# Kernel tuning notes

Measured on AMD Instinct MI355X. Metric: run time of the kernel, lower is better.

Reference implementation:

```python
import jax, jax.numpy as jnp
import numpy as np

NUM_STATES = 4096
NUM_OBS = 128
SEQ_LEN = 1024


def setup_inputs() -> dict:
    key = jax.random.key(0)
    kA, kB, kpi, kobs = jax.random.split(key, 4)
    # Scale A by 1/sqrt(N) so the forward recursion is numerically stable
    # (norm-preserving matvec); this only changes the random parameter draw,
    # not the math of the module.
    A = jax.random.normal(kA, (NUM_STATES, NUM_STATES), dtype=jnp.float32) / np.sqrt(NUM_STATES).astype(np.float32)
    B = jax.random.normal(kB, (NUM_STATES, NUM_OBS), dtype=jnp.float32)
    pi = jax.random.normal(kpi, (NUM_STATES,), dtype=jnp.float32)
    obs = jax.random.randint(kobs, (SEQ_LEN,), 0, NUM_OBS, dtype=jnp.int64)
    return {"A": A, "B": B, "pi": pi, "obs": obs}


def reference(A, B, pi, obs):
    # Gather the emission column for every timestep up front: (T, N)
    Bo = B[:, obs].T
    alpha0 = pi * Bo[0]  # (N,)

    def step(alpha, b_t):
        # alpha @ A : (N,) contracted with (N, N) -> (N,), then elementwise emission
        return (alpha @ A) * b_t, None

    alpha, _ = jax.lax.scan(step, alpha0, Bo[1:])
    return alpha.sum()
```

## Files before the change

kernel.cpp:

```cpp
#include <hip/hip_runtime.h>

constexpr int NSTATE = 4096;
constexpr int NOBS   = 128;
constexpr int TSEQ   = 1024;
constexpr int NWG    = 256;
constexpr int NTHR   = 1024;

constexpr size_t WS_BT    = 0;
constexpr size_t WS_OBS   = (size_t)NOBS * NSTATE;
constexpr size_t WS_FLAGS = WS_OBS + TSEQ;
constexpr size_t WS_Y2E   = WS_FLAGS + 512;

constexpr int XPAD = 20;

__device__ __forceinline__ int agent_ld_i32(const int* p) {
  return __hip_atomic_load(p, __ATOMIC_RELAXED, __HIP_MEMORY_SCOPE_AGENT);
}
__device__ __forceinline__ void agent_st_i32(int* p, int v) {
  __hip_atomic_store(p, v, __ATOMIC_RELAXED, __HIP_MEMORY_SCOPE_AGENT);
}
__device__ __forceinline__ void agent_st_f32(float* p, float v) {
  __hip_atomic_store(p, v, __ATOMIC_RELAXED, __HIP_MEMORY_SCOPE_AGENT);
}
__device__ __forceinline__ unsigned long long agent_ld_u64(const unsigned long long* p) {
  return __hip_atomic_load(p, __ATOMIC_RELAXED, __HIP_MEMORY_SCOPE_AGENT);
}
__device__ __forceinline__ void agent_st_u64(unsigned long long* p, unsigned long long v) {
  __hip_atomic_store(p, v, __ATOMIC_RELAXED, __HIP_MEMORY_SCOPE_AGENT);
}

__device__ __forceinline__ void grid_bar_full(int* flags, int w, int tid, int epoch) {
  asm volatile("s_waitcnt vmcnt(0)" ::: "memory");
  __syncthreads();
  if (tid == 0) agent_st_i32(&flags[w], epoch);
  if (tid < 64) {
    for (;;) {
      int m0 = agent_ld_i32(&flags[tid]);
      int m1 = agent_ld_i32(&flags[tid + 64]);
      int m2 = agent_ld_i32(&flags[tid + 128]);
      int m3 = agent_ld_i32(&flags[tid + 192]);
      int mn = min(min(m0, m1), min(m2, m3));
      if (__all(mn >= epoch)) break;
    }
  }
  __syncthreads();
}

__global__ __launch_bounds__(NTHR, 4) void hmm_fwd_kernel(
    const float* __restrict__ A,
    const float* __restrict__ B,
    const float* __restrict__ pi,
    const void*  __restrict__ obs_raw,
    float* __restrict__ out,
    float* __restrict__ ws)
{
  const int tid = threadIdx.x;
  const int w   = blockIdx.x;

  float* __restrict__ Bt    = ws + WS_BT;
  int*   __restrict__ obsg  = (int*)(ws + WS_OBS);
  int*   __restrict__ flags = (int*)(ws + WS_FLAGS);
  unsigned long long* __restrict__ y2e = (unsigned long long*)(ws + WS_Y2E);

  __shared__ float  x_lds[256 * XPAD];
  __shared__ float4 red_f[2][16][4];
  __shared__ int    obs_lds[TSEQ];
  __shared__ float  fin[16];
  __shared__ int    flag_lds;

  const int c4   = tid & 3;
  const int rg   = tid >> 2;
  const int ibase = rg << 4;
  const int col0  = (w << 4) + (c4 << 2);
  const int wave = tid >> 6;
  const int lane = tid & 63;

  const float* __restrict__ Abase = A + (size_t)ibase * NSTATE + col0;
  float ar[64];
#pragma unroll
  for (int k = 0; k < 16; ++k) {
    const float4 v = *(const float4*)(Abase + (size_t)k * NSTATE);
    ar[4*k+0] = v.x; ar[4*k+1] = v.y; ar[4*k+2] = v.z; ar[4*k+3] = v.w;
  }
#pragma unroll
  for (int i = 0; i < 64; ++i) asm volatile("" : "+v"(ar[i]));

  for (int e = w * NTHR + tid; e < NOBS * NSTATE; e += NWG * NTHR) {
    const int o = e >> 12;
    const int j = e & (NSTATE - 1);
    agent_st_f32(&Bt[(size_t)o * NSTATE + j], B[(size_t)j * NOBS + o]);
  }
  if (w == 0) {
    if (tid == 0) flag_lds = 0;
    __syncthreads();
    const long long* p64 = (const long long*)obs_raw;
    if (tid < 256) {
      const long long v = p64[tid];
      if (v < 0 || v >= NOBS) atomicOr(&flag_lds, 1);
    }
    __syncthreads();
    const bool is32 = (flag_lds != 0);
    const int* p32 = (const int*)obs_raw;
    agent_st_i32(&obsg[tid], is32 ? p32[tid] : (int)p64[tid]);
  }
  if (tid < 16) {
    union { float f; unsigned u; } cv;
    cv.f = pi[(w << 4) + tid];
    agent_st_u64(&y2e[(w << 4) + tid], (unsigned long long)cv.u);
  }
  grid_bar_full(flags, w, tid, 1);

  obs_lds[tid] = obsg[tid];
  __syncthreads();

  for (int t = 1; t < TSEQ; ++t) {
    const int bufc = (t - 1) & 1;
    const int bufp = t & 1;
    const int tagc = t - 1;
    const int o = obs_lds[t - 1];

    {
      const float4 bb = ((const float4*)(Bt + ((size_t)o << 12)))[tid];
      const unsigned long long* src = &y2e[(size_t)bufc * NSTATE + 4 * tid];
      unsigned long long v0, v1, v2, v3;
      for (;;) {
        v0 = agent_ld_u64(src + 0); v1 = agent_ld_u64(src + 1);
        v2 = agent_ld_u64(src + 2); v3 = agent_ld_u64(src + 3);
        bool ok = ((int)(v0 >> 32) == tagc) & ((int)(v1 >> 32) == tagc)
                & ((int)(v2 >> 32) == tagc) & ((int)(v3 >> 32) == tagc);
        if (ok) break;
      }
      union { unsigned u; float f; } e0, e1, e2, e3;
      e0.u = (unsigned)v0; e1.u = (unsigned)v1;
      e2.u = (unsigned)v2; e3.u = (unsigned)v3;
      float4 xx;
      xx.x = e0.f * bb.x; xx.y = e1.f * bb.y;
      xx.z = e2.f * bb.z; xx.w = e3.f * bb.w;
      *(float4*)(x_lds + (tid >> 2) * XPAD + (tid & 3) * 4) = xx;
    }
    __syncthreads();

    float acc0 = 0.f, acc1 = 0.f, acc2 = 0.f, acc3 = 0.f;
    {
      const float* xbase = x_lds + rg * XPAD;
#pragma unroll
      for (int q = 0; q < 4; ++q) {
        const float4 xv = *(const float4*)(xbase + 4 * q);
        const int k = 4 * q;
        acc0 = fmaf(xv.x, ar[4*(k+0)+0], acc0);
        acc1 = fmaf(xv.x, ar[4*(k+0)+1], acc1);
        acc2 = fmaf(xv.x, ar[4*(k+0)+2], acc2);
        acc3 = fmaf(xv.x, ar[4*(k+0)+3], acc3);
        acc0 = fmaf(xv.y, ar[4*(k+1)+0], acc0);
        acc1 = fmaf(xv.y, ar[4*(k+1)+1], acc1);
        acc2 = fmaf(xv.y, ar[4*(k+1)+2], acc2);
        acc3 = fmaf(xv.y, ar[4*(k+1)+3], acc3);
        acc0 = fmaf(xv.z, ar[4*(k+2)+0], acc0);
        acc1 = fmaf(xv.z, ar[4*(k+2)+1], acc1);
        acc2 = fmaf(xv.z, ar[4*(k+2)+2], acc2);
        acc3 = fmaf(xv.z, ar[4*(k+2)+3], acc3);
        acc0 = fmaf(xv.w, ar[4*(k+3)+0], acc0);
        acc1 = fmaf(xv.w, ar[4*(k+3)+1], acc1);
        acc2 = fmaf(xv.w, ar[4*(k+3)+2], acc2);
        acc3 = fmaf(xv.w, ar[4*(k+3)+3], acc3);
      }
    }
#pragma unroll
    for (int m = 4; m <= 32; m <<= 1) {
      acc0 += __shfl_xor(acc0, m);
      acc1 += __shfl_xor(acc1, m);
      acc2 += __shfl_xor(acc2, m);
      acc3 += __shfl_xor(acc3, m);
    }
    if ((lane >> 2) == 0) {
      red_f[bufp][wave][lane & 3] = make_float4(acc0, acc1, acc2, acc3);
    }
    __syncthreads();
    if (tid < 16) {
      float s = 0.f;
#pragma unroll
      for (int wv = 0; wv < 16; ++wv) {
        s += (&red_f[bufp][wv][tid >> 2].x)[tid & 3];
      }
      union { float f; unsigned u; } cv;
      cv.f = s;
      agent_st_u64(&y2e[(size_t)bufp * NSTATE + (w << 4) + tid],
                   ((unsigned long long)(unsigned)t << 32) | cv.u);
    }
  }

  if (w == 0) {
    const int o = obs_lds[TSEQ - 1];
    const int tagf = TSEQ - 1;
    const unsigned long long* src = &y2e[(size_t)1 * NSTATE + 4 * tid];
    const float* bo = Bt + ((size_t)o << 12) + 4 * tid;
    unsigned long long v0, v1, v2, v3;
    for (;;) {
      v0 = agent_ld_u64(src + 0); v1 = agent_ld_u64(src + 1);
      v2 = agent_ld_u64(src + 2); v3 = agent_ld_u64(src + 3);
      bool ok = ((int)(v0 >> 32) == tagf) & ((int)(v1 >> 32) == tagf)
              & ((int)(v2 >> 32) == tagf) & ((int)(v3 >> 32) == tagf);
      if (ok) break;
    }
    union { unsigned u; float f; } c0, c1, c2, c3;
    c0.u = (unsigned)v0; c1.u = (unsigned)v1; c2.u = (unsigned)v2; c3.u = (unsigned)v3;
    float s = c0.f * bo[0] + c1.f * bo[1] + c2.f * bo[2] + c3.f * bo[3];
#pragma unroll
    for (int m = 1; m <= 32; m <<= 1) s += __shfl_xor(s, m);
    if (lane == 0) fin[wave] = s;
    __syncthreads();
    if (tid == 0) {
      float tot = 0.f;
#pragma unroll
      for (int i = 0; i < 16; ++i) tot += fin[i];
      out[0] = tot;
    }
  }
}

extern "C" void kernel_launch(void* const* d_in, const int* in_sizes, int n_in,
                              void* d_out, int out_size, void* d_ws, size_t ws_size,
                              hipStream_t stream) {
  const float* A   = (const float*)d_in[0];
  const float* B   = (const float*)d_in[1];
  const float* pi  = (const float*)d_in[2];
  const void*  obs = d_in[3];
  float* out = (float*)d_out;
  float* ws  = (float*)d_ws;

  void* args[] = { &A, &B, &pi, &obs, &out, &ws };
  hipLaunchCooperativeKernel((void*)hmm_fwd_kernel, dim3(NWG), dim3(NTHR),
                             args, 0, stream);
}
```

Before: 4.315 ms.

## Replace tagged 64-bit value polling with per-workgroup flags plus bypass loads

Values were previously published as 64-bit words with a timestep tag, and every consumer thread spun on four such words. Now each workgroup writes plain floats, waits for them to complete, then sets a per-workgroup step flag. Consumers spin on the 16 relevant flags per wave and then read the data with a cache-bypassing dwordx4 load. This halves the polled data volume and reduces spin traffic, at the cost of an extra store-wait-flag handoff on the critical path of every step.

```diff
diff --git a/kernel.cpp b/kernel.cpp
--- a/kernel.cpp
+++ b/kernel.cpp
@@ -6,10 +6,11 @@
 constexpr int NWG    = 256;
 constexpr int NTHR   = 1024;
 
-constexpr size_t WS_BT    = 0;
-constexpr size_t WS_OBS   = (size_t)NOBS * NSTATE;
-constexpr size_t WS_FLAGS = WS_OBS + TSEQ;
-constexpr size_t WS_Y2E   = WS_FLAGS + 512;
+constexpr size_t WS_BT  = 0;
+constexpr size_t WS_OBS = (size_t)NOBS * NSTATE;
+constexpr size_t WS_BAR = WS_OBS + TSEQ;
+constexpr size_t WS_SFL = WS_BAR + 256;
+constexpr size_t WS_YF  = WS_SFL + 512;
 
 constexpr int XPAD = 20;
 
@@ -22,23 +23,25 @@
 __device__ __forceinline__ void agent_st_f32(float* p, float v) {
   __hip_atomic_store(p, v, __ATOMIC_RELAXED, __HIP_MEMORY_SCOPE_AGENT);
 }
-__device__ __forceinline__ unsigned long long agent_ld_u64(const unsigned long long* p) {
-  return __hip_atomic_load(p, __ATOMIC_RELAXED, __HIP_MEMORY_SCOPE_AGENT);
-}
-__device__ __forceinline__ void agent_st_u64(unsigned long long* p, unsigned long long v) {
-  __hip_atomic_store(p, v, __ATOMIC_RELAXED, __HIP_MEMORY_SCOPE_AGENT);
-}
-
-__device__ __forceinline__ void grid_bar_full(int* flags, int w, int tid, int epoch) {
+
+__device__ __forceinline__ float4 bypass_ld_f4(const float* p) {
+  float4 r;
+  asm volatile("global_load_dwordx4 %0, %1, off sc0 sc1\n\t"
+               "s_waitcnt vmcnt(0)"
+               : "=v"(r) : "v"(p) : "memory");
+  return r;
+}
+
+__device__ __forceinline__ void grid_bar_full(int* bar, int w, int tid, int epoch) {
   asm volatile("s_waitcnt vmcnt(0)" ::: "memory");
   __syncthreads();
-  if (tid == 0) agent_st_i32(&flags[w], epoch);
+  if (tid == 0) agent_st_i32(&bar[w], epoch);
   if (tid < 64) {
     for (;;) {
-      int m0 = agent_ld_i32(&flags[tid]);
-      int m1 = agent_ld_i32(&flags[tid + 64]);
-      int m2 = agent_ld_i32(&flags[tid + 128]);
-      int m3 = agent_ld_i32(&flags[tid + 192]);
+      int m0 = agent_ld_i32(&bar[tid]);
+      int m1 = agent_ld_i32(&bar[tid + 64]);
+      int m2 = agent_ld_i32(&bar[tid + 128]);
+      int m3 = agent_ld_i32(&bar[tid + 192]);
       int mn = min(min(m0, m1), min(m2, m3));
       if (__all(mn >= epoch)) break;
     }
@@ -57,10 +60,11 @@
   const int tid = threadIdx.x;
   const int w   = blockIdx.x;
 
-  float* __restrict__ Bt    = ws + WS_BT;
-  int*   __restrict__ obsg  = (int*)(ws + WS_OBS);
-  int*   __restrict__ flags = (int*)(ws + WS_FLAGS);
-  unsigned long long* __restrict__ y2e = (unsigned long long*)(ws + WS_Y2E);
+  float* __restrict__ Bt  = ws + WS_BT;
+  int*   __restrict__ obsg = (int*)(ws + WS_OBS);
+  int*   __restrict__ bar  = (int*)(ws + WS_BAR);
+  int*   __restrict__ sfl  = (int*)(ws + WS_SFL);
+  float* __restrict__ y_f  = ws + WS_YF;
 
   __shared__ float  x_lds[256 * XPAD];
   __shared__ float4 red_f[2][16][4];
@@ -74,6 +78,7 @@
   const int col0  = (w << 4) + (c4 << 2);
   const int wave = tid >> 6;
   const int lane = tid & 63;
+  const int row0 = tid << 2;
 
   const float* __restrict__ Abase = A + (size_t)ibase * NSTATE + col0;
   float ar[64];
@@ -104,11 +109,11 @@
     agent_st_i32(&obsg[tid], is32 ? p32[tid] : (int)p64[tid]);
   }
   if (tid < 16) {
-    union { float f; unsigned u; } cv;
-    cv.f = pi[(w << 4) + tid];
-    agent_st_u64(&y2e[(w << 4) + tid], (unsigned long long)cv.u);
-  }
-  grid_bar_full(flags, w, tid, 1);
+    agent_st_f32(&y_f[(w << 4) + tid], pi[(w << 4) + tid]);
+    asm volatile("s_waitcnt vmcnt(0)" ::: "memory");
+    if (tid == 0) agent_st_i32(&sfl[w], 0);
+  }
+  grid_bar_full(bar, w, tid, 1);
 
   obs_lds[tid] = obsg[tid];
   __syncthreads();
@@ -120,23 +125,17 @@
     const int o = obs_lds[t - 1];
 
     {
-      const float4 bb = ((const float4*)(Bt + ((size_t)o << 12)))[tid];
-      const unsigned long long* src = &y2e[(size_t)bufc * NSTATE + 4 * tid];
-      unsigned long long v0, v1, v2, v3;
+      const float4 bb = *(const float4*)(Bt + ((size_t)o << 12) + row0);
+      const int* fp = &sfl[bufc * 256 + (wave << 4) + (lane & 15)];
       for (;;) {
-        v0 = agent_ld_u64(src + 0); v1 = agent_ld_u64(src + 1);
-        v2 = agent_ld_u64(src + 2); v3 = agent_ld_u64(src + 3);
-        bool ok = ((int)(v0 >> 32) == tagc) & ((int)(v1 >> 32) == tagc)
-                & ((int)(v2 >> 32) == tagc) & ((int)(v3 >> 32) == tagc);
-        if (ok) break;
+        int f = agent_ld_i32(fp);
+        if (__all(f == tagc)) break;
       }
-      union { unsigned u; float f; } e0, e1, e2, e3;
-      e0.u = (unsigned)v0; e1.u = (unsigned)v1;
-      e2.u = (unsigned)v2; e3.u = (unsigned)v3;
+      const float4 yv = bypass_ld_f4(&y_f[(size_t)bufc * NSTATE + row0]);
       float4 xx;
-      xx.x = e0.f * bb.x; xx.y = e1.f * bb.y;
-      xx.z = e2.f * bb.z; xx.w = e3.f * bb.w;
-      *(float4*)(x_lds + (tid >> 2) * XPAD + (tid & 3) * 4) = xx;
+      xx.x = yv.x * bb.x; xx.y = yv.y * bb.y;
+      xx.z = yv.z * bb.z; xx.w = yv.w * bb.w;
+      *(float4*)(x_lds + (row0 >> 4) * XPAD + (row0 & 15)) = xx;
     }
     __syncthreads();
 
@@ -182,29 +181,23 @@
       for (int wv = 0; wv < 16; ++wv) {
         s += (&red_f[bufp][wv][tid >> 2].x)[tid & 3];
       }
-      union { float f; unsigned u; } cv;
-      cv.f = s;
-      agent_st_u64(&y2e[(size_t)bufp * NSTATE + (w << 4) + tid],
-                   ((unsigned long long)(unsigned)t << 32) | cv.u);
+      agent_st_f32(&y_f[(size_t)bufp * NSTATE + (w << 4) + tid], s);
+      asm volatile("s_waitcnt vmcnt(0)" ::: "memory");
+      if (tid == 0) agent_st_i32(&sfl[bufp * 256 + w], t);
     }
   }
 
   if (w == 0) {
     const int o = obs_lds[TSEQ - 1];
     const int tagf = TSEQ - 1;
-    const unsigned long long* src = &y2e[(size_t)1 * NSTATE + 4 * tid];
-    const float* bo = Bt + ((size_t)o << 12) + 4 * tid;
-    unsigned long long v0, v1, v2, v3;
+    const float4 bb = *(const float4*)(Bt + ((size_t)o << 12) + row0);
+    const int* fp = &sfl[1 * 256 + (wave << 4) + (lane & 15)];
     for (;;) {
-      v0 = agent_ld_u64(src + 0); v1 = agent_ld_u64(src + 1);
-      v2 = agent_ld_u64(src + 2); v3 = agent_ld_u64(src + 3);
-      bool ok = ((int)(v0 >> 32) == tagf) & ((int)(v1 >> 32) == tagf)
-              & ((int)(v2 >> 32) == tagf) & ((int)(v3 >> 32) == tagf);
-      if (ok) break;
-    }
-    union { unsigned u; float f; } c0, c1, c2, c3;
-    c0.u = (unsigned)v0; c1.u = (unsigned)v1; c2.u = (unsigned)v2; c3.u = (unsigned)v3;
-    float s = c0.f * bo[0] + c1.f * bo[1] + c2.f * bo[2] + c3.f * bo[3];
+      int f = agent_ld_i32(fp);
+      if (__all(f == tagf)) break;
+    }
+    const float4 yv = bypass_ld_f4(&y_f[(size_t)1 * NSTATE + row0]);
+    float s = yv.x * bb.x + yv.y * bb.y + yv.z * bb.z + yv.w * bb.w;
 #pragma unroll
     for (int m = 1; m <= 32; m <<= 1) s += __shfl_xor(s, m);
     if (lane == 0) fin[wave] = s;
```

Result: slower. 6.223 ms (+44.2%).

## Apply emission at producer and read tagged state directly, dropping LDS staging barrier

Applied to the files above, without the earlier changes.

The emission multiply moves from consumer to producer: each workgroup now scales its 16 output states by B[:,obs[t]] before publishing, so published values are already full alpha. Each thread then polls and reads exactly the four tagged alpha entries it needs straight from global memory using a swizzled layout, instead of all threads loading a float4, staging it through LDS and hitting a __syncthreads. This removes one block-wide barrier and the LDS round trip per timestep, and the per-thread ownership of rows changes to match. The cost is more scattered global atomic loads per thread, with each wave polling separately.

```diff
diff --git a/kernel.cpp b/kernel.cpp
--- a/kernel.cpp
+++ b/kernel.cpp
@@ -6,12 +6,10 @@
 constexpr int NWG    = 256;
 constexpr int NTHR   = 1024;
 
-constexpr size_t WS_BT    = 0;
-constexpr size_t WS_OBS   = (size_t)NOBS * NSTATE;
-constexpr size_t WS_FLAGS = WS_OBS + TSEQ;
-constexpr size_t WS_Y2E   = WS_FLAGS + 512;
-
-constexpr int XPAD = 20;
+constexpr size_t WS_BT  = 0;
+constexpr size_t WS_OBS = (size_t)NOBS * NSTATE;
+constexpr size_t WS_BAR = WS_OBS + TSEQ;
+constexpr size_t WS_Y2E = WS_BAR + 512;
 
 __device__ __forceinline__ int agent_ld_i32(const int* p) {
   return __hip_atomic_load(p, __ATOMIC_RELAXED, __HIP_MEMORY_SCOPE_AGENT);
@@ -19,6 +17,9 @@
 __device__ __forceinline__ void agent_st_i32(int* p, int v) {
   __hip_atomic_store(p, v, __ATOMIC_RELAXED, __HIP_MEMORY_SCOPE_AGENT);
 }
+__device__ __forceinline__ float agent_ld_f32(const float* p) {
+  return __hip_atomic_load(p, __ATOMIC_RELAXED, __HIP_MEMORY_SCOPE_AGENT);
+}
 __device__ __forceinline__ void agent_st_f32(float* p, float v) {
   __hip_atomic_store(p, v, __ATOMIC_RELAXED, __HIP_MEMORY_SCOPE_AGENT);
 }
@@ -29,16 +30,20 @@
   __hip_atomic_store(p, v, __ATOMIC_RELAXED, __HIP_MEMORY_SCOPE_AGENT);
 }
 
-__device__ __forceinline__ void grid_bar_full(int* flags, int w, int tid, int epoch) {
+__device__ __forceinline__ int swz(int c) {
+  return (c & ~255) | ((c >> 4) & 15) | ((c & 15) << 4);
+}
+
+__device__ __forceinline__ void grid_bar_full(int* bar, int w, int tid, int epoch) {
   asm volatile("s_waitcnt vmcnt(0)" ::: "memory");
   __syncthreads();
-  if (tid == 0) agent_st_i32(&flags[w], epoch);
+  if (tid == 0) agent_st_i32(&bar[w], epoch);
   if (tid < 64) {
     for (;;) {
-      int m0 = agent_ld_i32(&flags[tid]);
-      int m1 = agent_ld_i32(&flags[tid + 64]);
-      int m2 = agent_ld_i32(&flags[tid + 128]);
-      int m3 = agent_ld_i32(&flags[tid + 192]);
+      int m0 = agent_ld_i32(&bar[tid]);
+      int m1 = agent_ld_i32(&bar[tid + 64]);
+      int m2 = agent_ld_i32(&bar[tid + 128]);
+      int m3 = agent_ld_i32(&bar[tid + 192]);
       int mn = min(min(m0, m1), min(m2, m3));
       if (__all(mn >= epoch)) break;
     }
@@ -57,23 +62,22 @@
   const int tid = threadIdx.x;
   const int w   = blockIdx.x;
 
-  float* __restrict__ Bt    = ws + WS_BT;
-  int*   __restrict__ obsg  = (int*)(ws + WS_OBS);
-  int*   __restrict__ flags = (int*)(ws + WS_FLAGS);
+  float* __restrict__ Bt   = ws + WS_BT;
+  int*   __restrict__ obsg = (int*)(ws + WS_OBS);
+  int*   __restrict__ bar  = (int*)(ws + WS_BAR);
   unsigned long long* __restrict__ y2e = (unsigned long long*)(ws + WS_Y2E);
 
-  __shared__ float  x_lds[256 * XPAD];
   __shared__ float4 red_f[2][16][4];
   __shared__ int    obs_lds[TSEQ];
   __shared__ float  fin[16];
   __shared__ int    flag_lds;
 
   const int c4   = tid & 3;
-  const int rg   = tid >> 2;
-  const int ibase = rg << 4;
-  const int col0  = (w << 4) + (c4 << 2);
   const int wave = tid >> 6;
   const int lane = tid & 63;
+  const int q16  = lane >> 2;
+  const int ibase = (wave << 8) + (q16 << 4);
+  const int col0  = (w << 4) + (c4 << 2);
 
   const float* __restrict__ Abase = A + (size_t)ibase * NSTATE + col0;
   float ar[64];
@@ -103,66 +107,64 @@
     const int* p32 = (const int*)obs_raw;
     agent_st_i32(&obsg[tid], is32 ? p32[tid] : (int)p64[tid]);
   }
+  grid_bar_full(bar, w, tid, 1);
+
+  obs_lds[tid] = agent_ld_i32(&obsg[tid]);
+  __syncthreads();
+
   if (tid < 16) {
+    const int c = (w << 4) + tid;
     union { float f; unsigned u; } cv;
-    cv.f = pi[(w << 4) + tid];
-    agent_st_u64(&y2e[(w << 4) + tid], (unsigned long long)cv.u);
-  }
-  grid_bar_full(flags, w, tid, 1);
-
-  obs_lds[tid] = obsg[tid];
-  __syncthreads();
+    cv.f = pi[c] * agent_ld_f32(&Bt[((size_t)obs_lds[0] << 12) + c]);
+    agent_st_u64(&y2e[swz(c)], (unsigned long long)cv.u);
+  }
 
   for (int t = 1; t < TSEQ; ++t) {
     const int bufc = (t - 1) & 1;
     const int bufp = t & 1;
     const int tagc = t - 1;
-    const int o = obs_lds[t - 1];
-
-    {
-      const float4 bb = ((const float4*)(Bt + ((size_t)o << 12)))[tid];
-      const unsigned long long* src = &y2e[(size_t)bufc * NSTATE + 4 * tid];
-      unsigned long long v0, v1, v2, v3;
-      for (;;) {
-        v0 = agent_ld_u64(src + 0); v1 = agent_ld_u64(src + 1);
-        v2 = agent_ld_u64(src + 2); v3 = agent_ld_u64(src + 3);
-        bool ok = ((int)(v0 >> 32) == tagc) & ((int)(v1 >> 32) == tagc)
-                & ((int)(v2 >> 32) == tagc) & ((int)(v3 >> 32) == tagc);
-        if (ok) break;
-      }
-      union { unsigned u; float f; } e0, e1, e2, e3;
-      e0.u = (unsigned)v0; e1.u = (unsigned)v1;
-      e2.u = (unsigned)v2; e3.u = (unsigned)v3;
-      float4 xx;
-      xx.x = e0.f * bb.x; xx.y = e1.f * bb.y;
-      xx.z = e2.f * bb.z; xx.w = e3.f * bb.w;
-      *(float4*)(x_lds + (tid >> 2) * XPAD + (tid & 3) * 4) = xx;
-    }
-    __syncthreads();
+
+    float btn = 0.f;
+    if (tid < 16) {
+      btn = agent_ld_f32(&Bt[((size_t)obs_lds[t] << 12) + (w << 4) + tid]);
+    }
 
     float acc0 = 0.f, acc1 = 0.f, acc2 = 0.f, acc3 = 0.f;
     {
-      const float* xbase = x_lds + rg * XPAD;
-#pragma unroll
-      for (int q = 0; q < 4; ++q) {
-        const float4 xv = *(const float4*)(xbase + 4 * q);
-        const int k = 4 * q;
-        acc0 = fmaf(xv.x, ar[4*(k+0)+0], acc0);
-        acc1 = fmaf(xv.x, ar[4*(k+0)+1], acc1);
-        acc2 = fmaf(xv.x, ar[4*(k+0)+2], acc2);
-        acc3 = fmaf(xv.x, ar[4*(k+0)+3], acc3);
-        acc0 = fmaf(xv.y, ar[4*(k+1)+0], acc0);
-        acc1 = fmaf(xv.y, ar[4*(k+1)+1], acc1);
-        acc2 = fmaf(xv.y, ar[4*(k+1)+2], acc2);
-        acc3 = fmaf(xv.y, ar[4*(k+1)+3], acc3);
-        acc0 = fmaf(xv.z, ar[4*(k+2)+0], acc0);
-        acc1 = fmaf(xv.z, ar[4*(k+2)+1], acc1);
-        acc2 = fmaf(xv.z, ar[4*(k+2)+2], acc2);
-        acc3 = fmaf(xv.z, ar[4*(k+2)+3], acc3);
-        acc0 = fmaf(xv.w, ar[4*(k+3)+0], acc0);
-        acc1 = fmaf(xv.w, ar[4*(k+3)+1], acc1);
-        acc2 = fmaf(xv.w, ar[4*(k+3)+2], acc2);
-        acc3 = fmaf(xv.w, ar[4*(k+3)+3], acc3);
+      const unsigned long long* src =
+          &y2e[(size_t)bufc * NSTATE + (wave << 8) + q16];
+#pragma unroll
+      for (int g = 0; g < 4; ++g) {
+        unsigned long long v0, v1, v2, v3;
+        for (;;) {
+          v0 = agent_ld_u64(src + (g << 6) + 0);
+          v1 = agent_ld_u64(src + (g << 6) + 16);
+          v2 = agent_ld_u64(src + (g << 6) + 32);
+          v3 = agent_ld_u64(src + (g << 6) + 48);
+          bool ok = ((int)(v0 >> 32) == tagc) & ((int)(v1 >> 32) == tagc)
+                  & ((int)(v2 >> 32) == tagc) & ((int)(v3 >> 32) == tagc);
+          if (ok) break;
+        }
+        union { unsigned u; float f; } e0, e1, e2, e3;
+        e0.u = (unsigned)v0; e1.u = (unsigned)v1;
+        e2.u = (unsigned)v2; e3.u = (unsigned)v3;
+        const int k = g << 2;
+        acc0 = fmaf(e0.f, ar[4*(k+0)+0], acc0);
+        acc1 = fmaf(e0.f, ar[4*(k+0)+1], acc1);
+        acc2 = fmaf(e0.f, ar[4*(k+0)+2], acc2);
+        acc3 = fmaf(e0.f, ar[4*(k+0)+3], acc3);
+        acc0 = fmaf(e1.f, ar[4*(k+1)+0], acc0);
+        acc1 = fmaf(e1.f, ar[4*(k+1)+1], acc1);
+        acc2 = fmaf(e1.f, ar[4*(k+1)+2], acc2);
+        acc3 = fmaf(e1.f, ar[4*(k+1)+3], acc3);
+        acc0 = fmaf(e2.f, ar[4*(k+2)+0], acc0);
+        acc1 = fmaf(e2.f, ar[4*(k+2)+1], acc1);
+        acc2 = fmaf(e2.f, ar[4*(k+2)+2], acc2);
+        acc3 = fmaf(e2.f, ar[4*(k+2)+3], acc3);
+        acc0 = fmaf(e3.f, ar[4*(k+3)+0], acc0);
+        acc1 = fmaf(e3.f, ar[4*(k+3)+1], acc1);
+        acc2 = fmaf(e3.f, ar[4*(k+3)+2], acc2);
+        acc3 = fmaf(e3.f, ar[4*(k+3)+3], acc3);
       }
     }
 #pragma unroll
@@ -172,7 +174,7 @@
       acc2 += __shfl_xor(acc2, m);
       acc3 += __shfl_xor(acc3, m);
     }
-    if ((lane >> 2) == 0) {
+    if (q16 == 0) {
       red_f[bufp][wave][lane & 3] = make_float4(acc0, acc1, acc2, acc3);
     }
     __syncthreads();
@@ -182,18 +184,17 @@
       for (int wv = 0; wv < 16; ++wv) {
         s += (&red_f[bufp][wv][tid >> 2].x)[tid & 3];
       }
+      s *= btn;
       union { float f; unsigned u; } cv;
       cv.f = s;
-      agent_st_u64(&y2e[(size_t)bufp * NSTATE + (w << 4) + tid],
+      agent_st_u64(&y2e[(size_t)bufp * NSTATE + swz((w << 4) + tid)],
                    ((unsigned long long)(unsigned)t << 32) | cv.u);
     }
   }
 
   if (w == 0) {
-    const int o = obs_lds[TSEQ - 1];
     const int tagf = TSEQ - 1;
     const unsigned long long* src = &y2e[(size_t)1 * NSTATE + 4 * tid];
-    const float* bo = Bt + ((size_t)o << 12) + 4 * tid;
     unsigned long long v0, v1, v2, v3;
     for (;;) {
       v0 = agent_ld_u64(src + 0); v1 = agent_ld_u64(src + 1);
@@ -204,7 +205,7 @@
     }
     union { unsigned u; float f; } c0, c1, c2, c3;
     c0.u = (unsigned)v0; c1.u = (unsigned)v1; c2.u = (unsigned)v2; c3.u = (unsigned)v3;
-    float s = c0.f * bo[0] + c1.f * bo[1] + c2.f * bo[2] + c3.f * bo[3];
+    float s = c0.f + c1.f + c2.f + c3.f;
 #pragma unroll
     for (int m = 1; m <= 32; m <<= 1) s += __shfl_xor(s, m);
     if (lane == 0) fin[wave] = s;
```

New measurement: 5.840 ms. +35.4%, slower.
